# Optimization experiments

Hardware: AMD Instinct MI355X
Metric: run time of the kernel (lower is better)

Reference implementation:

```python
import jax, jax.numpy as jnp
import numpy as np

LN_EPS = 1e-5

def layernorm(x, w, b):
    # LayerNorm over last dim (head_dim), affine
    mu = jnp.mean(x, axis=-1, keepdims=True)
    var = jnp.mean(jnp.square(x - mu), axis=-1, keepdims=True)
    return (x - mu) * jax.lax.rsqrt(var + LN_EPS) * w + b

def setup_inputs() -> dict:
    key = jax.random.key(0)
    ks = jax.random.split(key, 6)
    B, N, C, H = 2, 2048, 1024, 16
    hd = C // H
    s = 1.0 / np.sqrt(C)
    return {
        "x": jax.random.normal(ks[0], (B, N, C), jnp.float32),
        "W_qkv": jax.random.normal(ks[1], (C, 3 * C), jnp.float32) * s,  # qkv_bias=False
        "qn_w": jnp.ones((hd,), jnp.float32),
        "qn_b": jnp.zeros((hd,), jnp.float32),
        "kn_w": jnp.ones((hd,), jnp.float32),
        "kn_b": jnp.zeros((hd,), jnp.float32),
        "W_proj": jax.random.normal(ks[2], (C, C), jnp.float32) * s,
        "b_proj": jnp.zeros((C,), jnp.float32),
    }

def reference(x, W_qkv, qn_w, qn_b, kn_w, kn_b, W_proj, b_proj):
    B, N, C = x.shape
    H = 16
    hd = C // H
    scale = hd ** -0.5
    qkv = (x @ W_qkv).reshape(B, N, 3, H, hd)
    qkv = jnp.transpose(qkv, (2, 0, 3, 1, 4))  # [3,B,H,N,hd]
    q, k, v = qkv[0], qkv[1], qkv[2]
    q = layernorm(q, qn_w, qn_b)
    k = layernorm(k, kn_w, kn_b)
    q = q * scale
    attn = jnp.einsum('bhnd,bhmd->bhnm', q, k)  # [B,H,N,N]
    attn = jax.nn.softmax(attn, axis=-1)  # attn_drop p=0 -> identity
    o = jnp.einsum('bhnm,bhmd->bhnd', attn, v)
    o = jnp.transpose(o, (0, 2, 1, 3)).reshape(B, N, C)
    return o @ W_proj + b_proj  # proj_drop p=0 -> identity
```

## Files before the change

### kernel.cpp

```cpp
#include <hip/hip_runtime.h>
#include <hip/hip_bf16.h>

#define B_  2
#define N_  2048
#define C_  1024
#define H_  16
#define HD_ 64
#define QSZ (B_*N_*C_)
#define QSCALE 0.18033688011112042f

typedef __attribute__((ext_vector_type(8))) short short8;
typedef __attribute__((ext_vector_type(4))) float floatx4;
typedef __attribute__((ext_vector_type(4))) unsigned short ushort4v;

__device__ __forceinline__ unsigned short f2bf(float f) {
    unsigned int u = __builtin_bit_cast(unsigned int, f);
    u += 0x7fff + ((u >> 16) & 1);
    return (unsigned short)(u >> 16);
}
__device__ __forceinline__ float bf2f(unsigned short h) {
    return __builtin_bit_cast(float, (unsigned int)h << 16);
}
__device__ __forceinline__ unsigned int pk2bf(float a, float b) {
    unsigned int ua = __builtin_bit_cast(unsigned int, a);
    unsigned int ub = __builtin_bit_cast(unsigned int, b);
    ua += 0x7fff + ((ua >> 16) & 1);
    ub += 0x7fff + ((ub >> 16) & 1);
    return __builtin_amdgcn_perm(ub, ua, 0x07060302);
}

__device__ __forceinline__ void g2l16(const void* g, void* l) {
    __builtin_amdgcn_global_load_lds(
        (const __attribute__((address_space(1))) void*)g,
        (__attribute__((address_space(3))) void*)l, 16, 0, 0);
}

__global__ __launch_bounds__(256) void pack_bf16_kernel(
    const float* __restrict__ src, unsigned short* __restrict__ dst)
{
    const int i = blockIdx.x * 256 + threadIdx.x;
    float4 v = ((const float4*)src)[i];
    ushort4 o = {f2bf(v.x), f2bf(v.y), f2bf(v.z), f2bf(v.w)};
    ((ushort4*)dst)[i] = o;
}

__global__ __launch_bounds__(256) void transpose_pack_kernel(
    const float* __restrict__ W, unsigned short* __restrict__ Wt,
    int Kd, int Nd)
{
    __shared__ unsigned short tl[32][34];
    const int r  = threadIdx.x >> 3;
    const int c4 = (threadIdx.x & 7) * 4;
    const int n0 = blockIdx.x * 32, k0 = blockIdx.y * 32;
    float4 v = *(const float4*)&W[(size_t)(k0 + r) * Nd + n0 + c4];
    tl[r][c4 + 0] = f2bf(v.x); tl[r][c4 + 1] = f2bf(v.y);
    tl[r][c4 + 2] = f2bf(v.z); tl[r][c4 + 3] = f2bf(v.w);
    __syncthreads();
    ushort4 o = {tl[c4 + 0][r], tl[c4 + 1][r], tl[c4 + 2][r], tl[c4 + 3][r]};
    *(ushort4*)&Wt[(size_t)(n0 + r) * Kd + k0 + c4] = o;
}

#define GEMM_CORE(A_, Bt_, Kd_, row0_, col0_)                                 \
    __shared__ unsigned short As[128 * 32];                                   \
    __shared__ unsigned short Bs[128 * 32];                                   \
    const int t    = threadIdx.x;                                             \
    const int lane = t & 63;                                                  \
    const int w    = t >> 6;                                                  \
    const int l15  = lane & 15;                                               \
    const int quad = lane >> 4;                                               \
    const int wm   = w >> 1, wn = w & 1;                                      \
    size_t aOff = (size_t)(row0_ + w * 16 + (lane >> 2)) * Kd_ + (lane & 3) * 8; \
    size_t bOff = (size_t)(col0_ + w * 16 + (lane >> 2)) * Kd_ + (lane & 3) * 8; \
    floatx4 acc[4][4];                                                        \
    _Pragma("unroll")                                                         \
    for (int i = 0; i < 4; ++i)                                               \
        _Pragma("unroll")                                                     \
        for (int j = 0; j < 4; ++j) acc[i][j] = floatx4{0.f, 0.f, 0.f, 0.f};  \
    for (int k0 = 0; k0 < Kd_; k0 += 32) {                                    \
        _Pragma("unroll")                                                     \
        for (int c = 0; c < 2; ++c) {                                         \
            g2l16(&A_[aOff + (size_t)c * 64 * Kd_ + k0],                      \
                  &As[(w * 16 + c * 64) * 32]);                               \
            g2l16(&Bt_[bOff + (size_t)c * 64 * Kd_ + k0],                     \
                  &Bs[(w * 16 + c * 64) * 32]);                               \
        }                                                                     \
        __syncthreads();                                                      \
        short8 af[4], bf[4];                                                  \
        _Pragma("unroll")                                                     \
        for (int i = 0; i < 4; ++i)                                           \
            af[i] = *(const short8*)&As[(wm * 64 + i * 16 + l15) * 32 + quad * 8]; \
        _Pragma("unroll")                                                     \
        for (int j = 0; j < 4; ++j)                                           \
            bf[j] = *(const short8*)&Bs[(wn * 64 + j * 16 + l15) * 32 + quad * 8]; \
        _Pragma("unroll")                                                     \
        for (int i = 0; i < 4; ++i)                                           \
            _Pragma("unroll")                                                 \
            for (int j = 0; j < 4; ++j)                                       \
                acc[i][j] = __builtin_amdgcn_mfma_f32_16x16x32_bf16(          \
                    af[i], bf[j], acc[i][j], 0, 0, 0);                        \
        __syncthreads();                                                      \
    }

__global__ __launch_bounds__(256) void gemm_qkv_kernel(
    const unsigned short* __restrict__ X,
    const unsigned short* __restrict__ Wt,
    const float* __restrict__ qn_w, const float* __restrict__ qn_b,
    const float* __restrict__ kn_w, const float* __restrict__ kn_b,
    unsigned short* __restrict__ qb, unsigned short* __restrict__ kb,
    unsigned short* __restrict__ vb)
{
    const int row0 = blockIdx.y * 128;
    const int col0 = blockIdx.x * 128;
    GEMM_CORE(X, Wt, 1024, row0, col0)
    const int which = col0 >> 10;
    const int h = ((col0 & 1023) >> 6) + wn;
    if (which == 2) {
        #pragma unroll
        for (int j = 0; j < 4; ++j) {
            const int d = j * 16 + l15;
            #pragma unroll
            for (int i = 0; i < 4; ++i) {
                #pragma unroll
                for (int r = 0; r < 4; ++r) {
                    const int grow = row0 + wm * 64 + i * 16 + quad * 4 + r;
                    const int bidx = grow >> 11, n = grow & 2047;
                    vb[(((size_t)(bidx * H_ + h) * N_ + n) * HD_) + d] =
                        f2bf(acc[i][j][r]);
                }
            }
        }
    } else {
        const float* wt = (which == 0) ? qn_w : kn_w;
        const float* bi = (which == 0) ? qn_b : kn_b;
        unsigned short* dstbuf = (which == 0) ? qb : kb;
        float w4[4], b4[4];
        #pragma unroll
        for (int j = 0; j < 4; ++j) {
            w4[j] = wt[j * 16 + l15];
            b4[j] = bi[j * 16 + l15];
        }
        #pragma unroll
        for (int i = 0; i < 4; ++i) {
            #pragma unroll
            for (int r = 0; r < 4; ++r) {
                float v0 = acc[i][0][r], v1 = acc[i][1][r],
                      v2 = acc[i][2][r], v3 = acc[i][3][r];
                float s = (v0 + v1) + (v2 + v3);
                #pragma unroll
                for (int o = 1; o < 16; o <<= 1) s += __shfl_xor(s, o);
                const float mu = s * (1.0f / 64.0f);
                const float d0 = v0 - mu, d1 = v1 - mu,
                            d2 = v2 - mu, d3 = v3 - mu;
                float s2 = (d0 * d0 + d1 * d1) + (d2 * d2 + d3 * d3);
                #pragma unroll
                for (int o = 1; o < 16; o <<= 1) s2 += __shfl_xor(s2, o);
                const float rstd = rsqrtf(s2 * (1.0f / 64.0f) + 1e-5f);
                float y0 = d0 * rstd * w4[0] + b4[0];
                float y1 = d1 * rstd * w4[1] + b4[1];
                float y2 = d2 * rstd * w4[2] + b4[2];
                float y3 = d3 * rstd * w4[3] + b4[3];
                if (which == 0) {
                    y0 *= QSCALE; y1 *= QSCALE; y2 *= QSCALE; y3 *= QSCALE;
                }
                const int grow = row0 + wm * 64 + i * 16 + quad * 4 + r;
                const int bidx = grow >> 11, n = grow & 2047;
                unsigned short* dp =
                    &dstbuf[(((size_t)(bidx * H_ + h) * N_ + n) * HD_) + l15];
                dp[0]  = f2bf(y0);
                dp[16] = f2bf(y1);
                dp[32] = f2bf(y2);
                dp[48] = f2bf(y3);
            }
        }
    }
}

__global__ __launch_bounds__(256) void gemm_proj_kernel(
    const unsigned short* __restrict__ O,
    const unsigned short* __restrict__ Wt,
    const float* __restrict__ bias, float* __restrict__ out)
{
    const int row0 = blockIdx.y * 128;
    const int col0 = blockIdx.x * 128;
    GEMM_CORE(O, Wt, 1024, row0, col0)
    #pragma unroll
    for (int j = 0; j < 4; ++j) {
        const int gcol = col0 + wn * 64 + j * 16 + l15;
        const float b = bias[gcol];
        #pragma unroll
        for (int i = 0; i < 4; ++i) {
            #pragma unroll
            for (int r = 0; r < 4; ++r) {
                const int grow = row0 + wm * 64 + i * 16 + quad * 4 + r;
                out[(size_t)grow * 1024 + gcol] = acc[i][j][r] + b;
            }
        }
    }
}

__global__ __launch_bounds__(512, 4) void flash_kernel(
    const unsigned short* __restrict__ qb, const unsigned short* __restrict__ kb,
    const unsigned short* __restrict__ vb, unsigned short* __restrict__ ob)
{
    __shared__ __align__(16) unsigned short Ks[128 * 72];
    __shared__ __align__(16) unsigned short Vt[64 * 136];
    __shared__ __align__(16) unsigned short Pb[128 * 136];
    const int t    = threadIdx.x;
    const int lane = t & 63;
    const int w    = t >> 6;
    const int l15  = lane & 15;
    const int quad = lane >> 4;
    const int q0   = blockIdx.x * 128;
    const int bh   = blockIdx.y;
    const unsigned short* Q = qb + (size_t)bh * N_ * HD_;
    const unsigned short* K = kb + (size_t)bh * N_ * HD_;
    const unsigned short* V = vb + (size_t)bh * N_ * HD_;

    {
        const int r = t >> 3, c = (t & 7) * 8;
        *(short8*)&Pb[r * 136 + c] =
            *(const short8*)&Q[(size_t)(q0 + r) * 64 + c];
        *(short8*)&Pb[(r + 64) * 136 + c] =
            *(const short8*)&Q[(size_t)(q0 + r + 64) * 64 + c];
    }
    __syncthreads();
    short8 qf[2];
    #pragma unroll
    for (int kk = 0; kk < 2; ++kk)
        qf[kk] = *(const short8*)&Pb[(w * 16 + l15) * 136 + kk * 32 + quad * 8];

    floatx4 acc[4];
    #pragma unroll
    for (int dt = 0; dt < 4; ++dt) acc[dt] = floatx4{0.f, 0.f, 0.f, 0.f};
    float l_part = 0.f;

    const int kr  = t >> 2, kc = (t & 3) * 16;
    const int vkv = (t & 63) * 2, vd = w * 8;

    short8 kA = *(const short8*)&K[(size_t)kr * 64 + kc];
    short8 kB = *(const short8*)&K[(size_t)kr * 64 + kc + 8];
    short8 vA = *(const short8*)&V[(size_t)vkv * 64 + vd];
    short8 vB = *(const short8*)&V[(size_t)(vkv + 1) * 64 + vd];

    for (int kt = 0; kt < N_; kt += 128) {
        __syncthreads();
        *(short8*)&Ks[kr * 72 + kc]     = kA;
        *(short8*)&Ks[kr * 72 + kc + 8] = kB;
        #pragma unroll
        for (int j = 0; j < 8; ++j) {
            unsigned int pk = (unsigned int)(unsigned short)vA[j] |
                              ((unsigned int)(unsigned short)vB[j] << 16);
            *(unsigned int*)&Vt[(vd + j) * 136 + vkv] = pk;
        }
        __syncthreads();
        if (kt + 128 < N_) {
            const int kt2 = kt + 128;
            kA = *(const short8*)&K[(size_t)(kt2 + kr) * 64 + kc];
            kB = *(const short8*)&K[(size_t)(kt2 + kr) * 64 + kc + 8];
            vA = *(const short8*)&V[(size_t)(kt2 + vkv) * 64 + vd];
            vB = *(const short8*)&V[(size_t)(kt2 + vkv + 1) * 64 + vd];
        }

        floatx4 sc[8];
        #pragma unroll
        for (int ct = 0; ct < 8; ++ct) {
            short8 a0 = *(const short8*)&Ks[(ct * 16 + l15) * 72 + quad * 8];
            short8 a1 = *(const short8*)&Ks[(ct * 16 + l15) * 72 + 32 + quad * 8];
            floatx4 r = {0.f, 0.f, 0.f, 0.f};
            r = __builtin_amdgcn_mfma_f32_16x16x32_bf16(a0, qf[0], r, 0, 0, 0);
            r = __builtin_amdgcn_mfma_f32_16x16x32_bf16(a1, qf[1], r, 0, 0, 0);
            sc[ct] = r;
        }

        const int prow = w * 16 + l15;
        #pragma unroll
        for (int ct = 0; ct < 8; ++ct) {
            float p0 = __builtin_amdgcn_exp2f(sc[ct][0]);
            float p1 = __builtin_amdgcn_exp2f(sc[ct][1]);
            float p2 = __builtin_amdgcn_exp2f(sc[ct][2]);
            float p3 = __builtin_amdgcn_exp2f(sc[ct][3]);
            l_part += (p0 + p1) + (p2 + p3);
            uint2 pk;
            pk.x = pk2bf(p0, p1);
            pk.y = pk2bf(p2, p3);
            *(uint2*)&Pb[prow * 136 + ct * 16 + quad * 4] = pk;
        }
        asm volatile("" ::: "memory");

        #pragma unroll
        for (int kk = 0; kk < 4; ++kk) {
            short8 pbf = *(const short8*)
                &Pb[(w * 16 + l15) * 136 + kk * 32 + quad * 8];
            #pragma unroll
            for (int dt = 0; dt < 4; ++dt) {
                short8 va = *(const short8*)
                    &Vt[(dt * 16 + l15) * 136 + kk * 32 + quad * 8];
                acc[dt] = __builtin_amdgcn_mfma_f32_16x16x32_bf16(
                    va, pbf, acc[dt], 0, 0, 0);
            }
        }
    }

    l_part += __shfl_xor(l_part, 16);
    l_part += __shfl_xor(l_part, 32);

    asm volatile("" ::: "memory");
    {
        const float inv = 1.0f / l_part;
        const int orow = w * 16 + l15;
        #pragma unroll
        for (int dt = 0; dt < 4; ++dt) {
            uint2 o2;
            o2.x = pk2bf(acc[dt][0] * inv, acc[dt][1] * inv);
            o2.y = pk2bf(acc[dt][2] * inv, acc[dt][3] * inv);
            *(uint2*)&Pb[orow * 136 + dt * 16 + quad * 4] = o2;
        }
    }
    __syncthreads();
    const int bidx = bh >> 4, h = bh & 15;
    {
        const int r = t >> 3, c = (t & 7) * 8;
        *(short8*)&ob[((size_t)(bidx * N_ + q0 + r)) * C_ + h * 64 + c] =
            *(const short8*)&Pb[r * 136 + c];
        *(short8*)&ob[((size_t)(bidx * N_ + q0 + r + 64)) * C_ + h * 64 + c] =
            *(const short8*)&Pb[(r + 64) * 136 + c];
    }
}

extern "C" void kernel_launch(void* const* d_in, const int* in_sizes, int n_in,
                              void* d_out, int out_size, void* d_ws, size_t ws_size,
                              hipStream_t stream) {
    const float* x      = (const float*)d_in[0];
    const float* W_qkv  = (const float*)d_in[1];
    const float* qn_w   = (const float*)d_in[2];
    const float* qn_b   = (const float*)d_in[3];
    const float* kn_w   = (const float*)d_in[4];
    const float* kn_b   = (const float*)d_in[5];
    const float* W_proj = (const float*)d_in[6];
    const float* b_proj = (const float*)d_in[7];
    float* out = (float*)d_out;

    unsigned short* qb  = (unsigned short*)d_ws;
    unsigned short* kb  = qb + (size_t)QSZ;
    unsigned short* vb  = kb + (size_t)QSZ;
    unsigned short* ob  = vb + (size_t)QSZ;
    unsigned short* xb  = ob + (size_t)B_ * N_ * C_;
    unsigned short* wqt = xb + (size_t)B_ * N_ * C_;
    unsigned short* wpt = wqt + (size_t)3 * C_ * C_;

    pack_bf16_kernel<<<dim3((B_ * N_ * C_) / 1024), 256, 0, stream>>>(x, xb);
    transpose_pack_kernel<<<dim3(96, 32), 256, 0, stream>>>(W_qkv, wqt, 1024, 3072);
    transpose_pack_kernel<<<dim3(32, 32), 256, 0, stream>>>(W_proj, wpt, 1024, 1024);
    gemm_qkv_kernel<<<dim3(24, 32), 256, 0, stream>>>(
        xb, wqt, qn_w, qn_b, kn_w, kn_b, qb, kb, vb);
    flash_kernel<<<dim3(N_ / 128, B_ * H_), 512, 0, stream>>>(qb, kb, vb, ob);
    gemm_proj_kernel<<<dim3(8, 32), 256, 0, stream>>>(ob, wpt, b_proj, out);
}
```

Before: 204.7 us.

## Restructure flash kernel to 4 waves with two query groups, retile proj GEMM, merge weight packs

The flash kernel now runs 256 threads instead of 512. Each wave handles two 16-row query groups, so every K and V fragment read from LDS is reused across both groups, halving LDS traffic per MFMA. The projection GEMM switches to 64x128 tiles, doubling the grid to 512 blocks for better CU fill. The two weight transpose-pack launches are merged into one to save a launch. In exchange, each thread in the flash kernel holds more accumulator registers and there are fewer waves to hide latency.

Result: no change. 202.9 us (-0.9%).

```diff
diff --git a/kernel.cpp b/kernel.cpp
--- a/kernel.cpp
+++ b/kernel.cpp
@@ -44,20 +44,25 @@
     ((ushort4*)dst)[i] = o;
 }
 
-__global__ __launch_bounds__(256) void transpose_pack_kernel(
-    const float* __restrict__ W, unsigned short* __restrict__ Wt,
-    int Kd, int Nd)
+__global__ __launch_bounds__(256) void transpose_pack2_kernel(
+    const float* __restrict__ Wq, unsigned short* __restrict__ Wqt,
+    const float* __restrict__ Wp, unsigned short* __restrict__ Wpt)
 {
     __shared__ unsigned short tl[32][34];
+    const bool isq = blockIdx.x < 96;
+    const int bx = isq ? blockIdx.x : blockIdx.x - 96;
+    const int Nd = isq ? 3072 : 1024;
+    const float* W = isq ? Wq : Wp;
+    unsigned short* Wt = isq ? Wqt : Wpt;
     const int r  = threadIdx.x >> 3;
     const int c4 = (threadIdx.x & 7) * 4;
-    const int n0 = blockIdx.x * 32, k0 = blockIdx.y * 32;
+    const int n0 = bx * 32, k0 = blockIdx.y * 32;
     float4 v = *(const float4*)&W[(size_t)(k0 + r) * Nd + n0 + c4];
     tl[r][c4 + 0] = f2bf(v.x); tl[r][c4 + 1] = f2bf(v.y);
     tl[r][c4 + 2] = f2bf(v.z); tl[r][c4 + 3] = f2bf(v.w);
     __syncthreads();
     ushort4 o = {tl[c4 + 0][r], tl[c4 + 1][r], tl[c4 + 2][r], tl[c4 + 3][r]};
-    *(ushort4*)&Wt[(size_t)(n0 + r) * Kd + k0 + c4] = o;
+    *(ushort4*)&Wt[(size_t)(n0 + r) * 1024 + k0 + c4] = o;
 }
 
 #define GEMM_CORE(A_, Bt_, Kd_, row0_, col0_)                                 \
@@ -180,25 +185,60 @@
     const unsigned short* __restrict__ Wt,
     const float* __restrict__ bias, float* __restrict__ out)
 {
-    const int row0 = blockIdx.y * 128;
+    __shared__ unsigned short As[64 * 32];
+    __shared__ unsigned short Bs[128 * 32];
+    const int t    = threadIdx.x;
+    const int lane = t & 63;
+    const int w    = t >> 6;
+    const int l15  = lane & 15;
+    const int quad = lane >> 4;
+    const int row0 = blockIdx.y * 64;
     const int col0 = blockIdx.x * 128;
-    GEMM_CORE(O, Wt, 1024, row0, col0)
-    #pragma unroll
-    for (int j = 0; j < 4; ++j) {
-        const int gcol = col0 + wn * 64 + j * 16 + l15;
+    size_t aOff = (size_t)(row0 + w * 16 + (lane >> 2)) * 1024 + (lane & 3) * 8;
+    size_t bOff = (size_t)(col0 + w * 16 + (lane >> 2)) * 1024 + (lane & 3) * 8;
+    floatx4 acc[4][2];
+    #pragma unroll
+    for (int i = 0; i < 4; ++i)
+        #pragma unroll
+        for (int j = 0; j < 2; ++j) acc[i][j] = floatx4{0.f, 0.f, 0.f, 0.f};
+    for (int k0 = 0; k0 < 1024; k0 += 32) {
+        g2l16(&O[aOff + k0], &As[(w * 16) * 32]);
+        #pragma unroll
+        for (int c = 0; c < 2; ++c)
+            g2l16(&Wt[bOff + (size_t)c * 64 * 1024 + k0],
+                  &Bs[(w * 16 + c * 64) * 32]);
+        __syncthreads();
+        short8 af[4], bf[2];
+        #pragma unroll
+        for (int i = 0; i < 4; ++i)
+            af[i] = *(const short8*)&As[(i * 16 + l15) * 32 + quad * 8];
+        #pragma unroll
+        for (int j = 0; j < 2; ++j)
+            bf[j] = *(const short8*)&Bs[(w * 32 + j * 16 + l15) * 32 + quad * 8];
+        #pragma unroll
+        for (int i = 0; i < 4; ++i)
+            #pragma unroll
+            for (int j = 0; j < 2; ++j)
+                acc[i][j] = __builtin_amdgcn_mfma_f32_16x16x32_bf16(
+                    af[i], bf[j], acc[i][j], 0, 0, 0);
+        __syncthreads();
+    }
+    #pragma unroll
+    for (int j = 0; j < 2; ++j) {
+        const int gcol = col0 + w * 32 + j * 16 + l15;
         const float b = bias[gcol];
         #pragma unroll
         for (int i = 0; i < 4; ++i) {
             #pragma unroll
             for (int r = 0; r < 4; ++r) {
-                const int grow = row0 + wm * 64 + i * 16 + quad * 4 + r;
+                const int grow = row0 + i * 16 + quad * 4 + r;
                 out[(size_t)grow * 1024 + gcol] = acc[i][j][r] + b;
             }
         }
     }
 }
 
-__global__ __launch_bounds__(512, 4) void flash_kernel(
+__global__ __launch_bounds__(256, 2) void flash_kernel(
     const unsigned short* __restrict__ qb, const unsigned short* __restrict__ kb,
     const unsigned short* __restrict__ vb, unsigned short* __restrict__ ob)
 {
@@ -218,101 +258,128 @@
 
     {
         const int r = t >> 3, c = (t & 7) * 8;
-        *(short8*)&Pb[r * 136 + c] =
-            *(const short8*)&Q[(size_t)(q0 + r) * 64 + c];
-        *(short8*)&Pb[(r + 64) * 136 + c] =
-            *(const short8*)&Q[(size_t)(q0 + r + 64) * 64 + c];
+        #pragma unroll
+        for (int rep = 0; rep < 4; ++rep)
+            *(short8*)&Pb[(rep * 32 + r) * 136 + c] =
+                *(const short8*)&Q[(size_t)(q0 + rep * 32 + r) * 64 + c];
     }
     __syncthreads();
-    short8 qf[2];
-    #pragma unroll
-    for (int kk = 0; kk < 2; ++kk)
-        qf[kk] = *(const short8*)&Pb[(w * 16 + l15) * 136 + kk * 32 + quad * 8];
-
-    floatx4 acc[4];
-    #pragma unroll
-    for (int dt = 0; dt < 4; ++dt) acc[dt] = floatx4{0.f, 0.f, 0.f, 0.f};
-    float l_part = 0.f;
-
-    const int kr  = t >> 2, kc = (t & 3) * 16;
-    const int vkv = (t & 63) * 2, vd = w * 8;
-
-    short8 kA = *(const short8*)&K[(size_t)kr * 64 + kc];
-    short8 kB = *(const short8*)&K[(size_t)kr * 64 + kc + 8];
-    short8 vA = *(const short8*)&V[(size_t)vkv * 64 + vd];
-    short8 vB = *(const short8*)&V[(size_t)(vkv + 1) * 64 + vd];
+    short8 qf[2][2];
+    #pragma unroll
+    for (int qg = 0; qg < 2; ++qg)
+        #pragma unroll
+        for (int kk = 0; kk < 2; ++kk)
+            qf[qg][kk] = *(const short8*)
+                &Pb[(qg * 64 + w * 16 + l15) * 136 + kk * 32 + quad * 8];
+
+    floatx4 acc[2][4];
+    #pragma unroll
+    for (int qg = 0; qg < 2; ++qg)
+        #pragma unroll
+        for (int dt = 0; dt < 4; ++dt) acc[qg][dt] = floatx4{0.f, 0.f, 0.f, 0.f};
+    float l_part[2] = {0.f, 0.f};
+
+    const int kr = t & 127, kc = (t >> 7) * 32;
+    const int vkv = (t & 63) * 2, vd = (t >> 6) * 16;
+
+    short8 kR[4], vR[4];
+    #pragma unroll
+    for (int c = 0; c < 4; ++c)
+        kR[c] = *(const short8*)&K[(size_t)kr * 64 + kc + c * 8];
+    vR[0] = *(const short8*)&V[(size_t)vkv * 64 + vd];
+    vR[1] = *(const short8*)&V[(size_t)vkv * 64 + vd + 8];
+    vR[2] = *(const short8*)&V[(size_t)(vkv + 1) * 64 + vd];
+    vR[3] = *(const short8*)&V[(size_t)(vkv + 1) * 64 + vd + 8];
 
     for (int kt = 0; kt < N_; kt += 128) {
         __syncthreads();
-        *(short8*)&Ks[kr * 72 + kc]     = kA;
-        *(short8*)&Ks[kr * 72 + kc + 8] = kB;
+        #pragma unroll
+        for (int c = 0; c < 4; ++c)
+            *(short8*)&Ks[kr * 72 + kc + c * 8] = kR[c];
         #pragma unroll
         for (int j = 0; j < 8; ++j) {
-            unsigned int pk = (unsigned int)(unsigned short)vA[j] |
-                              ((unsigned int)(unsigned short)vB[j] << 16);
-            *(unsigned int*)&Vt[(vd + j) * 136 + vkv] = pk;
+            unsigned int p0 = (unsigned int)(unsigned short)vR[0][j] |
+                              ((unsigned int)(unsigned short)vR[2][j] << 16);
+            unsigned int p1 = (unsigned int)(unsigned short)vR[1][j] |
+                              ((unsigned int)(unsigned short)vR[3][j] << 16);
+            *(unsigned int*)&Vt[(vd + j) * 136 + vkv]     = p0;
+            *(unsigned int*)&Vt[(vd + 8 + j) * 136 + vkv] = p1;
         }
         __syncthreads();
         if (kt + 128 < N_) {
             const int kt2 = kt + 128;
-            kA = *(const short8*)&K[(size_t)(kt2 + kr) * 64 + kc];
-            kB = *(const short8*)&K[(size_t)(kt2 + kr) * 64 + kc + 8];
-            vA = *(const short8*)&V[(size_t)(kt2 + vkv) * 64 + vd];
-            vB = *(const short8*)&V[(size_t)(kt2 + vkv + 1) * 64 + vd];
-        }
-
-        floatx4 sc[8];
+            #pragma unroll
+            for (int c = 0; c < 4; ++c)
+                kR[c] = *(const short8*)&K[(size_t)(kt2 + kr) * 64 + kc + c * 8];
+            vR[0] = *(const short8*)&V[(size_t)(kt2 + vkv) * 64 + vd];
+            vR[1] = *(const short8*)&V[(size_t)(kt2 + vkv) * 64 + vd + 8];
+            vR[2] = *(const short8*)&V[(size_t)(kt2 + vkv + 1) * 64 + vd];
+            vR[3] = *(const short8*)&V[(size_t)(kt2 + vkv + 1) * 64 + vd + 8];
+        }
+
+        floatx4 sc[2][8];
         #pragma unroll
         for (int ct = 0; ct < 8; ++ct) {
             short8 a0 = *(const short8*)&Ks[(ct * 16 + l15) * 72 + quad * 8];
             short8 a1 = *(const short8*)&Ks[(ct * 16 + l15) * 72 + 32 + quad * 8];
-            floatx4 r = {0.f, 0.f, 0.f, 0.f};
-            r = __builtin_amdgcn_mfma_f32_16x16x32_bf16(a0, qf[0], r, 0, 0, 0);
-            r = __builtin_amdgcn_mfma_f32_16x16x32_bf16(a1, qf[1], r, 0, 0, 0);
-            sc[ct] = r;
-        }
-
-        const int prow = w * 16 + l15;
-        #pragma unroll
-        for (int ct = 0; ct < 8; ++ct) {
-            float p0 = __builtin_amdgcn_exp2f(sc[ct][0]);
-            float p1 = __builtin_amdgcn_exp2f(sc[ct][1]);
-            float p2 = __builtin_amdgcn_exp2f(sc[ct][2]);
-            float p3 = __builtin_amdgcn_exp2f(sc[ct][3]);
-            l_part += (p0 + p1) + (p2 + p3);
-            uint2 pk;
-            pk.x = pk2bf(p0, p1);
-            pk.y = pk2bf(p2, p3);
-            *(uint2*)&Pb[prow * 136 + ct * 16 + quad * 4] = pk;
+            #pragma unroll
+            for (int qg = 0; qg < 2; ++qg) {
+                floatx4 r = {0.f, 0.f, 0.f, 0.f};
+                r = __builtin_amdgcn_mfma_f32_16x16x32_bf16(a0, qf[qg][0], r, 0, 0, 0);
+                r = __builtin_amdgcn_mfma_f32_16x16x32_bf16(a1, qf[qg][1], r, 0, 0, 0);
+                sc[qg][ct] = r;
+            }
+        }
+
+        #pragma unroll
+        for (int qg = 0; qg < 2; ++qg) {
+            const int prow = qg * 64 + w * 16 + l15;
+            #pragma unroll
+            for (int ct = 0; ct < 8; ++ct) {
+                float p0 = __builtin_amdgcn_exp2f(sc[qg][ct][0]);
+                float p1 = __builtin_amdgcn_exp2f(sc[qg][ct][1]);
+                float p2 = __builtin_amdgcn_exp2f(sc[qg][ct][2]);
+                float p3 = __builtin_amdgcn_exp2f(sc[qg][ct][3]);
+                l_part[qg] += (p0 + p1) + (p2 + p3);
+                uint2 pk;
+                pk.x = pk2bf(p0, p1);
+                pk.y = pk2bf(p2, p3);
+                *(uint2*)&Pb[prow * 136 + ct * 16 + quad * 4] = pk;
+            }
         }
         asm volatile("" ::: "memory");
 
         #pragma unroll
         for (int kk = 0; kk < 4; ++kk) {
-            short8 pbf = *(const short8*)
-                &Pb[(w * 16 + l15) * 136 + kk * 32 + quad * 8];
+            short8 pbf[2];
+            #pragma unroll
+            for (int qg = 0; qg < 2; ++qg)
+                pbf[qg] = *(const short8*)
+                    &Pb[(qg * 64 + w * 16 + l15) * 136 + kk * 32 + quad * 8];
             #pragma unroll
             for (int dt = 0; dt < 4; ++dt) {
                 short8 va = *(const short8*)
                     &Vt[(dt * 16 + l15) * 136 + kk * 32 + quad * 8];
-                acc[dt] = __builtin_amdgcn_mfma_f32_16x16x32_bf16(
-                    va, pbf, acc[dt], 0, 0, 0);
-            }
-        }
-    }
-
-    l_part += __shfl_xor(l_part, 16);
-    l_part += __shfl_xor(l_part, 32);
+                #pragma unroll
+                for (int qg = 0; qg < 2; ++qg)
+                    acc[qg][dt] = __builtin_amdgcn_mfma_f32_16x16x32_bf16(
+                        va, pbf[qg], acc[qg][dt], 0, 0, 0);
+            }
+        }
+    }
 
     asm volatile("" ::: "memory");
-    {
-        const float inv = 1.0f / l_part;
-        const int orow = w * 16 + l15;
+    #pragma unroll
+    for (int qg = 0; qg < 2; ++qg) {
+        l_part[qg] += __shfl_xor(l_part[qg], 16);
+        l_part[qg] += __shfl_xor(l_part[qg], 32);
+        const float inv = 1.0f / l_part[qg];
+        const int orow = qg * 64 + w * 16 + l15;
         #pragma unroll
         for (int dt = 0; dt < 4; ++dt) {
             uint2 o2;
-            o2.x = pk2bf(acc[dt][0] * inv, acc[dt][1] * inv);
-            o2.y = pk2bf(acc[dt][2] * inv, acc[dt][3] * inv);
+            o2.x = pk2bf(acc[qg][dt][0] * inv, acc[qg][dt][1] * inv);
+            o2.y = pk2bf(acc[qg][dt][2] * inv, acc[qg][dt][3] * inv);
             *(uint2*)&Pb[orow * 136 + dt * 16 + quad * 4] = o2;
         }
     }
@@ -320,10 +387,12 @@
     const int bidx = bh >> 4, h = bh & 15;
     {
         const int r = t >> 3, c = (t & 7) * 8;
-        *(short8*)&ob[((size_t)(bidx * N_ + q0 + r)) * C_ + h * 64 + c] =
-            *(const short8*)&Pb[r * 136 + c];
-        *(short8*)&ob[((size_t)(bidx * N_ + q0 + r + 64)) * C_ + h * 64 + c] =
-            *(const short8*)&Pb[(r + 64) * 136 + c];
+        #pragma unroll
+        for (int rep = 0; rep < 4; ++rep) {
+            const int row = rep * 32 + r;
+            *(short8*)&ob[((size_t)(bidx * N_ + q0 + row)) * C_ + h * 64 + c] =
+                *(const short8*)&Pb[row * 136 + c];
+        }
     }
 }
 
@@ -349,10 +418,9 @@
     unsigned short* wpt = wqt + (size_t)3 * C_ * C_;
 
     pack_bf16_kernel<<<dim3((B_ * N_ * C_) / 1024), 256, 0, stream>>>(x, xb);
-    transpose_pack_kernel<<<dim3(96, 32), 256, 0, stream>>>(W_qkv, wqt, 1024, 3072);
-    transpose_pack_kernel<<<dim3(32, 32), 256, 0, stream>>>(W_proj, wpt, 1024, 1024);
+    transpose_pack2_kernel<<<dim3(128, 32), 256, 0, stream>>>(W_qkv, wqt, W_proj, wpt);
     gemm_qkv_kernel<<<dim3(24, 32), 256, 0, stream>>>(
         xb, wqt, qn_w, qn_b, kn_w, kn_b, qb, kb, vb);
-    flash_kernel<<<dim3(N_ / 128, B_ * H_), 512, 0, stream>>>(qb, kb, vb, ob);
-    gemm_proj_kernel<<<dim3(8, 32), 256, 0, stream>>>(ob, wpt, b_proj, out);
-}
+    flash_kernel<<<dim3(N_ / 128, B_ * H_), 256, 0, stream>>>(qb, kb, vb, ob);
+    gemm_proj_kernel<<<dim3(8, 64), 256, 0, stream>>>(ob, wpt, b_proj, out);
+}
```
